# Optimization experiments

Measured on AMD Instinct MI355X. Metric: run time of the kernel, lower is better.

Reference implementation:

```python
import jax, jax.numpy as jnp
import numpy as np

OVERLAP_THRESHOLD = 0.8
NUM_CLASSES = 1  # class-agnostic: class 0 = thing, class 1 = no-object


def setup_inputs() -> dict:
    key = jax.random.key(0)
    k1, k2 = jax.random.split(key)
    B, P, Q = 2, 200000, 100
    mask_cls = jax.random.normal(k1, (B, Q, NUM_CLASSES + 1), dtype=jnp.float32)
    mask_pred = jax.random.normal(k2, (B, P, Q), dtype=jnp.float32)
    pad = jnp.zeros((B, P), dtype=bool)  # no padded points -> static shapes
    return {"mask_cls": mask_cls, "mask_pred": mask_pred, "pad": pad}


def _panoptic_single(mask_cls, mask_pred):
    # mask_cls: [Q, C+1] logits, mask_pred: [P, Q] mask logits
    Q = mask_pred.shape[1]
    scores = mask_cls.max(-1)                     # [Q]
    labels = jnp.argmax(mask_cls, axis=-1)        # [Q]
    keep = labels != NUM_CLASSES                  # [Q] queries not predicted as no-object

    m = jax.nn.sigmoid(mask_pred)                 # [P, Q]
    # score-weighted masks; non-kept queries excluded via -inf (0 after softmax,
    # never selected by argmax) -- equivalent to torch's column subselection.
    prob = jnp.where(keep[None, :], scores[None, :] * m, -jnp.inf)  # [P, Q]
    probabilities = jax.nn.softmax(prob, axis=1)
    max_confs = probabilities.max(axis=1)         # [P]

    ids = jnp.argmax(prob, axis=1)                # [P] winning query per point
    ones = jnp.ones((mask_pred.shape[0],), dtype=jnp.int32)
    mask_area = jax.ops.segment_sum(ones, ids, num_segments=Q)      # (cur_mask_ids == k).sum()

    orig_bin = m >= 0.5                           # [P, Q]
    orig_area = orig_bin.astype(jnp.int32).sum(axis=0)              # (cur_masks[:, k] >= 0.5).sum()
    point_bin = jnp.take_along_axis(orig_bin, ids[:, None], axis=1)[:, 0]  # [P]
    mask_count = jax.ops.segment_sum(point_bin.astype(jnp.int32), ids, num_segments=Q)

    ratio = mask_area.astype(jnp.float32) / jnp.maximum(orig_area, 1).astype(jnp.float32)
    accepted = (keep & (mask_area > 0) & (orig_area > 0) & (mask_count > 0)
                & (ratio >= OVERLAP_THRESHOLD))   # [Q]

    # sequential segment_id assignment == cumulative count of accepted queries
    # (all queries are 'things'; masks are disjoint since they come from argmax)
    seg_id = jnp.where(accepted, jnp.cumsum(accepted.astype(jnp.int32)), 0)  # [Q]

    point_valid = accepted[ids] & point_bin       # [P] (cur_mask_ids==k) & (mask>=0.5) & accepted
    ins = jnp.where(point_valid, seg_id[ids], 0).astype(jnp.int32)
    sem = jnp.where(point_valid, labels[ids], 0).astype(jnp.int32)
    return sem, ins, max_confs


def reference(mask_cls, mask_pred, pad):
    # pad is all-False (no padded points), so mask_pred[~pad] is identity and
    # shapes stay static; pad is accepted for signature fidelity.
    del pad
    sem, ins, max_confs = jax.vmap(_panoptic_single)(mask_cls, mask_pred)
    return sem, ins, max_confs
```

## Files before the change

kernel.cpp:

```cpp
#include <hip/hip_runtime.h>
#include <cstdint>
#include <cstddef>

#define BB 2
#define PP 200000
#define QQ 100
#define TPB 256
#define PTS 64
#define NBX (PP / PTS)
#define QSL 28
#define QPAD 112
#define PITCH4 25
#define NSLICE 8


__device__ __forceinline__ void gload_lds16(const float4* g, float4* l) {
    __builtin_amdgcn_global_load_lds(
        (const __attribute__((address_space(1))) uint32_t*)g,
        (__attribute__((address_space(3))) uint32_t*)l,
        16, 0, 0);
}

__global__ __launch_bounds__(TPB, 4) void stats_kernel(
    const float* __restrict__ mask_cls,
    const float* __restrict__ mask_pred,
    float* __restrict__ out_conf,
    int* __restrict__ ws_ids,
    int* __restrict__ g_cnt)
{
    __shared__ float4 s_flat[PTS * PITCH4 + 8];
    __shared__ __attribute__((aligned(16))) float s_score[QPAD];
    __shared__ int s_cnt[3 * QQ];
    __shared__ float s_best[4][PTS];
    __shared__ float s_sum[4][PTS];
    __shared__ int s_id[4][PTS];

    const int b = blockIdx.y;
    const int t = threadIdx.x;
    const int lane = t & 63;
    const int w = t >> 6;

    if (t < QPAD) {
        float v = -INFINITY;
        if (t < QQ) {
            float c0 = mask_cls[(b * QQ + t) * 2 + 0];
            float c1 = mask_cls[(b * QQ + t) * 2 + 1];
            bool keep = !(c1 > c0);
            v = keep ? fmaxf(c0, c1) : -INFINITY;
        }
        s_score[t] = v;
    }
    for (int i = t; i < 3 * QQ; i += TPB) s_cnt[i] = 0;

    const float4* __restrict__ g = reinterpret_cast<const float4*>(
        mask_pred + ((size_t)b * PP + (size_t)blockIdx.x * PTS) * QQ);
#pragma unroll
    for (int k = 0; k < 6; ++k) {
        const int idx = (w + 4 * k) * 64 + lane;
        gload_lds16(g + idx, s_flat + idx);
    }
    if (w == 0) {
        const int idx = 24 * 64 + lane;
        gload_lds16(g + idx, s_flat + idx);
    }
    __syncthreads();

    const int p = blockIdx.x * PTS + lane;
    const int qoff = w * QSL;

    const float4* __restrict__ myrow = s_flat + lane * PITCH4 + w * 7;
    float4 r[7], scr[7];
#pragma unroll
    for (int i = 0; i < 7; ++i) r[i] = myrow[i];
    const float4* s_sc4 = reinterpret_cast<const float4*>(s_score + qoff);
#pragma unroll
    for (int i = 0; i < 7; ++i) scr[i] = s_sc4[i];

    float best = -INFINITY;
    float sumexp = 0.f;
    int bestid = 0;
    bool any = false;
    int corig = 0;

#pragma unroll
    for (int i = 0; i < 7; ++i) {
        const float4 x4 = r[i];
        const float4 s4 = scr[i];
        const float xs[4] = {x4.x, x4.y, x4.z, x4.w};
        const float ss[4] = {s4.x, s4.y, s4.z, s4.w};
#pragma unroll
        for (int c = 0; c < 4; ++c) {
            const int j = i * 4 + c;
            const float sc = ss[c];
            if (sc == -INFINITY) continue;

            float sig = 1.0f / (1.0f + expf(-xs[c]));
            const int bin = (sig >= 0.5f) ? 1 : 0;

            unsigned long long mb = __ballot(bin);
            corig += (lane == j) ? __popcll(mb) : 0;

            const float v = sc * fmaxf(sig, 1e-38f);
            sumexp += __expf(v);
            if (v > best) {
                best = v;
                bestid = (((qoff + j) << 1) | bin);
                any = true;
            }
        }
    }

    const int qlen = (w == 3) ? (QQ - 3 * QSL) : QSL;
    if (lane < qlen) atomicAdd(&s_cnt[qoff + lane], corig);

    s_best[w][lane] = best;
    s_sum[w][lane] = sumexp;
    s_id[w][lane] = any ? bestid : 0;
    __syncthreads();

    if (w == 0) {
        float bb = s_best[0][lane];
        float se = s_sum[0][lane];
        int id = s_id[0][lane];
#pragma unroll
        for (int ww = 1; ww < 4; ++ww) {
            const float b2 = s_best[ww][lane];
            se += s_sum[ww][lane];
            if (b2 > bb) { bb = b2; id = s_id[ww][lane]; }
        }
        const int q = id >> 1, bin = id & 1;
        atomicAdd(&s_cnt[QQ + q], 1);
        if (bin) atomicAdd(&s_cnt[2 * QQ + q], 1);
        out_conf[(size_t)b * PP + p] = __expf(bb) / se;
        ws_ids[(size_t)b * PP + p] = id;
    }
    __syncthreads();

    {
        const int slice = blockIdx.x & (NSLICE - 1);
        int* gc = g_cnt + (slice * BB + b) * 3 * QQ;
        for (int i = t; i < 3 * QQ; i += TPB)
            if (s_cnt[i]) atomicAdd(&gc[i], s_cnt[i]);
    }
}

#define STPB 1024
#define SNBX ((PP / 4 + STPB - 1) / STPB)

__global__ __launch_bounds__(STPB) void scatter_kernel(
    const float* __restrict__ mask_cls,
    const int* __restrict__ g_cnt,
    const int* __restrict__ ws_ids,
    float* __restrict__ out_sem,
    float* __restrict__ out_ins)
{
    __shared__ int s_acc[QQ], s_lab[QQ];
    __shared__ float s_sem[QQ], s_ins[QQ];
    const int b = blockIdx.y;
    const int t = threadIdx.x;

    if (t < QQ) {
        float c0 = mask_cls[(b * QQ + t) * 2 + 0];
        float c1 = mask_cls[(b * QQ + t) * 2 + 1];
        bool keep = !(c1 > c0);
        int oa = 0, ma = 0, mc = 0;
#pragma unroll
        for (int s = 0; s < NSLICE; ++s) {
            const int* gc = g_cnt + (s * BB + b) * 3 * QQ;
            oa += gc[t]; ma += gc[QQ + t]; mc += gc[2 * QQ + t];
        }
        float ratio = (float)ma / (float)max(oa, 1);
        bool acc = keep && (ma > 0) && (oa > 0) && (mc > 0) && (ratio >= 0.8f);
        s_acc[t] = acc ? 1 : 0;
        s_lab[t] = (c1 > c0) ? 1 : 0;
    }
    __syncthreads();
    if (t == 0) {
        int run = 0;
        for (int q = 0; q < QQ; ++q) {
            int a = s_acc[q];
            run += a;
            s_sem[q] = a ? (float)s_lab[q] : 0.0f;
            s_ins[q] = a ? (float)run : 0.0f;
        }
    }
    __syncthreads();

    const int i4 = blockIdx.x * STPB + t;
    if (i4 < PP / 4) {
        const int4 v = reinterpret_cast<const int4*>(ws_ids + (size_t)b * PP)[i4];
        const int vv[4] = {v.x, v.y, v.z, v.w};
        float se[4], in[4];
#pragma unroll
        for (int k = 0; k < 4; ++k) {
            const int bin = vv[k] & 1;
            const int q = vv[k] >> 1;
            se[k] = bin ? s_sem[q] : 0.0f;
            in[k] = bin ? s_ins[q] : 0.0f;
        }
        reinterpret_cast<float4*>(out_sem + (size_t)b * PP)[i4] =
            make_float4(se[0], se[1], se[2], se[3]);
        reinterpret_cast<float4*>(out_ins + (size_t)b * PP)[i4] =
            make_float4(in[0], in[1], in[2], in[3]);
    }
}

extern "C" void kernel_launch(void* const* d_in, const int* in_sizes, int n_in,
                              void* d_out, int out_size, void* d_ws, size_t ws_size,
                              hipStream_t stream) {
    const float* mask_cls  = (const float*)d_in[0];
    const float* mask_pred = (const float*)d_in[1];

    float* out = (float*)d_out;
    int* ws = (int*)d_ws;
    int* g_cnt  = ws;
    int* ws_ids = g_cnt + NSLICE * BB * 3 * QQ;

    hipMemsetAsync(g_cnt, 0, NSLICE * BB * 3 * QQ * sizeof(int), stream);

    stats_kernel<<<dim3(NBX, BB), TPB, 0, stream>>>(
        mask_cls, mask_pred, out + 2 * (size_t)BB * PP, ws_ids, g_cnt);
    scatter_kernel<<<dim3(SNBX, BB), STPB, 0, stream>>>(
        mask_cls, g_cnt, ws_ids, out, out + (size_t)BB * PP);
}
```

Before: 240.6 us.

## Make stats kernel persistent with double-buffered LDS prefetch of tiles

The stats kernel becomes a persistent grid of 256 blocks per batch. Each block loops over point tiles, issuing the async global-to-LDS loads for the next tile into a second LDS buffer before it computes on the current one. The aim is to hide global load latency behind the sigmoid, exp and argmax work and to cut per-block launch and setup cost. In exchange, the doubled LDS buffer and the lowered launch-bounds occupancy hint leave fewer resident waves to hide latency. The barrier inside the loop may also force the prefetch to finish early in each iteration, which limits how much overlap is actually gained.

```diff
diff --git a/kernel.cpp b/kernel.cpp
--- a/kernel.cpp
+++ b/kernel.cpp
@@ -8,9 +8,11 @@
 #define TPB 256
 #define PTS 64
 #define NBX (PP / PTS)
+#define GRIDX 256
 #define QSL 28
 #define QPAD 112
-#define PITCH4 25
+#define ROW4 25
+#define TILE4 (PTS * ROW4)
 #define NSLICE 8
 
 
@@ -21,14 +23,14 @@
         16, 0, 0);
 }
 
-__global__ __launch_bounds__(TPB, 4) void stats_kernel(
+__global__ __launch_bounds__(TPB, 2) void stats_kernel(
     const float* __restrict__ mask_cls,
     const float* __restrict__ mask_pred,
     float* __restrict__ out_conf,
     int* __restrict__ ws_ids,
     int* __restrict__ g_cnt)
 {
-    __shared__ float4 s_flat[PTS * PITCH4 + 8];
+    __shared__ float4 s_flat[2][TILE4 + 8];
     __shared__ __attribute__((aligned(16))) float s_score[QPAD];
     __shared__ int s_cnt[3 * QQ];
     __shared__ float s_best[4][PTS];
@@ -39,6 +41,23 @@
     const int t = threadIdx.x;
     const int lane = t & 63;
     const int w = t >> 6;
+    const int bx = blockIdx.x;
+
+    const float4* __restrict__ gbase = reinterpret_cast<const float4*>(
+        mask_pred + (size_t)b * PP * QQ);
+
+    {
+        const float4* g = gbase + (size_t)bx * TILE4;
+#pragma unroll
+        for (int k = 0; k < 6; ++k) {
+            const int idx = (w + 4 * k) * 64 + lane;
+            gload_lds16(g + idx, &s_flat[0][idx]);
+        }
+        if (w == 0) {
+            const int idx = 24 * 64 + lane;
+            gload_lds16(g + idx, &s_flat[0][idx]);
+        }
+    }
 
     if (t < QPAD) {
         float v = -INFINITY;
@@ -51,93 +70,100 @@
         s_score[t] = v;
     }
     for (int i = t; i < 3 * QQ; i += TPB) s_cnt[i] = 0;
-
-    const float4* __restrict__ g = reinterpret_cast<const float4*>(
-        mask_pred + ((size_t)b * PP + (size_t)blockIdx.x * PTS) * QQ);
-#pragma unroll
-    for (int k = 0; k < 6; ++k) {
-        const int idx = (w + 4 * k) * 64 + lane;
-        gload_lds16(g + idx, s_flat + idx);
-    }
-    if (w == 0) {
-        const int idx = 24 * 64 + lane;
-        gload_lds16(g + idx, s_flat + idx);
-    }
     __syncthreads();
 
-    const int p = blockIdx.x * PTS + lane;
     const int qoff = w * QSL;
-
-    const float4* __restrict__ myrow = s_flat + lane * PITCH4 + w * 7;
-    float4 r[7], scr[7];
-#pragma unroll
-    for (int i = 0; i < 7; ++i) r[i] = myrow[i];
     const float4* s_sc4 = reinterpret_cast<const float4*>(s_score + qoff);
+    float4 scr[7];
 #pragma unroll
     for (int i = 0; i < 7; ++i) scr[i] = s_sc4[i];
-
-    float best = -INFINITY;
-    float sumexp = 0.f;
-    int bestid = 0;
-    bool any = false;
-    int corig = 0;
-
-#pragma unroll
-    for (int i = 0; i < 7; ++i) {
-        const float4 x4 = r[i];
-        const float4 s4 = scr[i];
-        const float xs[4] = {x4.x, x4.y, x4.z, x4.w};
-        const float ss[4] = {s4.x, s4.y, s4.z, s4.w};
-#pragma unroll
-        for (int c = 0; c < 4; ++c) {
-            const int j = i * 4 + c;
-            const float sc = ss[c];
-            if (sc == -INFINITY) continue;
-
-            float sig = 1.0f / (1.0f + expf(-xs[c]));
-            const int bin = (sig >= 0.5f) ? 1 : 0;
-
-            unsigned long long mb = __ballot(bin);
-            corig += (lane == j) ? __popcll(mb) : 0;
-
-            const float v = sc * fmaxf(sig, 1e-38f);
-            sumexp += __expf(v);
-            if (v > best) {
-                best = v;
-                bestid = (((qoff + j) << 1) | bin);
-                any = true;
-            }
-        }
-    }
-
     const int qlen = (w == 3) ? (QQ - 3 * QSL) : QSL;
-    if (lane < qlen) atomicAdd(&s_cnt[qoff + lane], corig);
-
-    s_best[w][lane] = best;
-    s_sum[w][lane] = sumexp;
-    s_id[w][lane] = any ? bestid : 0;
-    __syncthreads();
-
-    if (w == 0) {
-        float bb = s_best[0][lane];
-        float se = s_sum[0][lane];
-        int id = s_id[0][lane];
-#pragma unroll
-        for (int ww = 1; ww < 4; ++ww) {
-            const float b2 = s_best[ww][lane];
-            se += s_sum[ww][lane];
-            if (b2 > bb) { bb = b2; id = s_id[ww][lane]; }
-        }
-        const int q = id >> 1, bin = id & 1;
-        atomicAdd(&s_cnt[QQ + q], 1);
-        if (bin) atomicAdd(&s_cnt[2 * QQ + q], 1);
-        out_conf[(size_t)b * PP + p] = __expf(bb) / se;
-        ws_ids[(size_t)b * PP + p] = id;
-    }
-    __syncthreads();
+
+    int cur = 0;
+    for (int tile = bx; tile < NBX; tile += GRIDX) {
+        const int nxt = tile + GRIDX;
+        if (nxt < NBX) {
+            const float4* g = gbase + (size_t)nxt * TILE4;
+            float4* dst = s_flat[cur ^ 1];
+#pragma unroll
+            for (int k = 0; k < 6; ++k) {
+                const int idx = (w + 4 * k) * 64 + lane;
+                gload_lds16(g + idx, dst + idx);
+            }
+            if (w == 0) {
+                const int idx = 24 * 64 + lane;
+                gload_lds16(g + idx, dst + idx);
+            }
+        }
+
+        const float4* myrow = s_flat[cur] + lane * ROW4 + w * 7;
+        float4 r[7];
+#pragma unroll
+        for (int i = 0; i < 7; ++i) r[i] = myrow[i];
+
+        float best = -INFINITY;
+        float sumexp = 0.f;
+        int bestid = 0;
+        bool any = false;
+        int corig = 0;
+
+#pragma unroll
+        for (int i = 0; i < 7; ++i) {
+            const float4 x4 = r[i];
+            const float4 s4 = scr[i];
+            const float xs[4] = {x4.x, x4.y, x4.z, x4.w};
+            const float ss[4] = {s4.x, s4.y, s4.z, s4.w};
+#pragma unroll
+            for (int c = 0; c < 4; ++c) {
+                const int j = i * 4 + c;
+                const float sc = ss[c];
+                if (sc == -INFINITY) continue;
+
+                float sig = 1.0f / (1.0f + expf(-xs[c]));
+                const int bin = (sig >= 0.5f) ? 1 : 0;
+
+                unsigned long long mb = __ballot(bin);
+                corig += (lane == j) ? __popcll(mb) : 0;
+
+                const float v = sc * fmaxf(sig, 1e-38f);
+                sumexp += __expf(v);
+                if (v > best) {
+                    best = v;
+                    bestid = (((qoff + j) << 1) | bin);
+                    any = true;
+                }
+            }
+        }
+
+        if (lane < qlen) atomicAdd(&s_cnt[qoff + lane], corig);
+        s_best[w][lane] = best;
+        s_sum[w][lane] = sumexp;
+        s_id[w][lane] = any ? bestid : 0;
+        __syncthreads();
+
+        if (w == 0) {
+            float bb = s_best[0][lane];
+            float se = s_sum[0][lane];
+            int id = s_id[0][lane];
+#pragma unroll
+            for (int ww = 1; ww < 4; ++ww) {
+                const float b2 = s_best[ww][lane];
+                se += s_sum[ww][lane];
+                if (b2 > bb) { bb = b2; id = s_id[ww][lane]; }
+            }
+            const int q = id >> 1, bin = id & 1;
+            atomicAdd(&s_cnt[QQ + q], 1);
+            if (bin) atomicAdd(&s_cnt[2 * QQ + q], 1);
+            const int p = tile * PTS + lane;
+            out_conf[(size_t)b * PP + p] = __expf(bb) / se;
+            ws_ids[(size_t)b * PP + p] = id;
+        }
+        __syncthreads();
+        cur ^= 1;
+    }
 
     {
-        const int slice = blockIdx.x & (NSLICE - 1);
+        const int slice = bx & (NSLICE - 1);
         int* gc = g_cnt + (slice * BB + b) * 3 * QQ;
         for (int i = t; i < 3 * QQ; i += TPB)
             if (s_cnt[i]) atomicAdd(&gc[i], s_cnt[i]);
@@ -218,7 +244,7 @@
 
     hipMemsetAsync(g_cnt, 0, NSLICE * BB * 3 * QQ * sizeof(int), stream);
 
-    stats_kernel<<<dim3(NBX, BB), TPB, 0, stream>>>(
+    stats_kernel<<<dim3(GRIDX, BB), TPB, 0, stream>>>(
         mask_cls, mask_pred, out + 2 * (size_t)BB * PP, ws_ids, g_cnt);
     scatter_kernel<<<dim3(SNBX, BB), STPB, 0, stream>>>(
         mask_cls, g_cnt, ws_ids, out, out + (size_t)BB * PP);
```

Measured after the change: 244.5 us. No clear change (+1.6%).
